# Kernel optimization log

Hardware: AMD Instinct MI355X
Metric: run time of the kernel (lower is better)

The kernel has to match this reference:

```python
import jax, jax.numpy as jnp
import numpy as np


def _hilbert_d2xy(n, d):
    # standard Hilbert curve: distance d -> (x, y) on n x n grid (n power of 2)
    x = y = 0
    t = d
    s = 1
    while s < n:
        rx = 1 & (t // 2)
        ry = 1 & (t ^ rx)
        if ry == 0:
            if rx == 1:
                x = s - 1 - x
                y = s - 1 - y
            x, y = y, x
        x += s * rx
        y += s * ry
        t //= 4
        s *= 2
    return x, y


def _hilbert_perm(seq_len):
    n = int(round(np.sqrt(seq_len)))
    assert n * n == seq_len
    perm = np.empty(seq_len, dtype=np.int32)
    for d in range(seq_len):
        x, y = _hilbert_d2xy(n, d)
        perm[d] = y * n + x  # linear (row-major) index visited at Hilbert step d
    return perm


def setup_inputs() -> dict:
    key = jax.random.key(0)
    k1, k2, k3 = jax.random.split(key, 3)
    B, S, H, D = 1, 4096, 8, 64
    q = jax.random.normal(k1, (B, S, H, D), dtype=jnp.float32)
    k = jax.random.normal(k2, (B, S, H, D), dtype=jnp.float32)
    v = jax.random.normal(k3, (B, S, H, D), dtype=jnp.float32)
    hilbert_perm = jnp.asarray(_hilbert_perm(S))
    return {"q": q, "k": k, "v": v, "hilbert_perm": hilbert_perm}


def reference(q, k, v, hilbert_perm):
    B, S, H, D = q.shape
    inv_perm = jnp.argsort(hilbert_perm)

    # apply_hilbert_ordering along dim=1 (seq): gather by permutation
    q_o = q[:, hilbert_perm]
    k_o = k[:, hilbert_perm]
    v_o = v[:, hilbert_perm]

    # faithful to original: raw flat reshape of [B,S,H,D] -> [B*H, S, D]
    q_f = q_o.reshape(B * H, S, D)
    k_f = k_o.reshape(B * H, S, D)
    v_f = v_o.reshape(B * H, S, D)

    scale = 1.0 / jnp.sqrt(jnp.asarray(D, dtype=q.dtype))
    scores = jnp.einsum('bsd,btd->bst', q_f, k_f) * scale  # [B*H, S, S]
    attn = jax.nn.softmax(scores, axis=-1)
    out_f = jnp.einsum('bst,btd->bsd', attn, v_f)  # [B*H, S, D]

    out = out_f.reshape(B, H, S, D).transpose(0, 2, 1, 3).reshape(B, S, H, D)
    # inverse Hilbert ordering along dim=1
    return out[:, inv_perm]
```

## Files before the change

### kernel.cpp

```cpp
#include <hip/hip_runtime.h>

typedef _Float16 f16;
typedef _Float16 f16x4 __attribute__((ext_vector_type(4)));
typedef _Float16 f16x8 __attribute__((ext_vector_type(8)));
typedef __fp16 fp16x2 __attribute__((ext_vector_type(2)));
typedef float f32x4 __attribute__((ext_vector_type(4)));

#define MFMA_16x16x32_F16(A, B, C) __builtin_amdgcn_mfma_f32_16x16x32_f16((A), (B), (C), 0, 0, 0)

typedef const __attribute__((address_space(1))) char gchar;
typedef __attribute__((address_space(3))) char lchar;

__device__ __forceinline__ float fexp2(float x) { return __builtin_amdgcn_exp2f(x); }
__device__ __forceinline__ int swzb(int b) { return b ^ ((b >> 3) & 0x70); }

namespace {
constexpr int SB = 4096;
constexpr size_t BB = (size_t)SB * 64 * 2;
}

__global__ __launch_bounds__(256)
void hilbert_prepass_kernel(const float* __restrict__ kp, const float* __restrict__ vp,
                            const int* __restrict__ perm,
                            char* __restrict__ kw, char* __restrict__ vtw)
{
    const int bid = blockIdx.x;
    const int batch = bid & 7;
    const int tile = bid >> 3;
    const int tid = (int)threadIdx.x;
    const int r = tid >> 2;
    const int c4 = tid & 3;

    __shared__ float Vl[64][68];

    const int t = tile * 64 + r;
    const int srow = perm[batch * 512 + (t >> 3)];
    const size_t boff = (size_t)srow * 512 + (t & 7) * 64 + c4 * 16;

    {
        const float* ks = kp + boff;
        const float4 k0 = *(const float4*)(ks + 0);
        const float4 k1 = *(const float4*)(ks + 4);
        const float4 k2 = *(const float4*)(ks + 8);
        const float4 k3 = *(const float4*)(ks + 12);
        f16x8 h0, h1;
        h0[0] = (f16)k0.x; h0[1] = (f16)k0.y; h0[2] = (f16)k0.z; h0[3] = (f16)k0.w;
        h0[4] = (f16)k1.x; h0[5] = (f16)k1.y; h0[6] = (f16)k1.z; h0[7] = (f16)k1.w;
        h1[0] = (f16)k2.x; h1[1] = (f16)k2.y; h1[2] = (f16)k2.z; h1[3] = (f16)k2.w;
        h1[4] = (f16)k3.x; h1[5] = (f16)k3.y; h1[6] = (f16)k3.z; h1[7] = (f16)k3.w;
        char* kt = kw + (size_t)batch * BB + (size_t)tile * 8192;
        const int o = r * 128 + c4 * 32;
        *(f16x8*)(kt + swzb(o)) = h0;
        *(f16x8*)(kt + swzb(o + 16)) = h1;
    }
    {
        const float* vs = vp + boff;
        *(float4*)&Vl[r][c4 * 16 + 0]  = *(const float4*)(vs + 0);
        *(float4*)&Vl[r][c4 * 16 + 4]  = *(const float4*)(vs + 4);
        *(float4*)&Vl[r][c4 * 16 + 8]  = *(const float4*)(vs + 8);
        *(float4*)&Vl[r][c4 * 16 + 12] = *(const float4*)(vs + 12);
    }
    __syncthreads();
    {
        const int d = tid >> 2;
        const int tq = (tid & 3) * 16;
        f16x8 a, b;
#pragma unroll
        for (int j = 0; j < 8; ++j) a[j] = (f16)Vl[tq + j][d];
#pragma unroll
        for (int j = 0; j < 8; ++j) b[j] = (f16)Vl[tq + 8 + j][d];
        char* vt = vtw + (size_t)batch * BB + (size_t)tile * 8192;
        const int o = d * 128 + tq * 2;
        *(f16x8*)(vt + swzb(o)) = a;
        *(f16x8*)(vt + swzb(o + 16)) = b;
    }
}

__global__ __launch_bounds__(512, 2)
void hilbert_attn_kernel(const float* __restrict__ qp,
                         const int* __restrict__ perm,
                         const char* __restrict__ kw, const char* __restrict__ vtw,
                         float* __restrict__ op)
{
    __shared__ __align__(16) char SM[98304];

    const int bid = blockIdx.x;
    const int batch = bid & 7;
    const int qbase = (bid >> 3) * 128;
    const int tid = (int)threadIdx.x;
    const int w = tid >> 6;
    const int lane = tid & 63;
    const int l16 = lane & 15;
    const int g = lane >> 4;
    const int half = w >> 2;
    const int wq = w & 3;
    const int swz = (l16 & 7) << 4;

    f16x8 Qf0[2], Qf1[2];
    {
        constexpr float qscl = 0.125f * 1.44269504088896340736f;
#pragma unroll
        for (int s = 0; s < 2; ++s) {
            const int t = qbase + wq * 32 + s * 16 + l16;
            const int srow = perm[batch * 512 + (t >> 3)];
            const float* src = qp + (size_t)srow * 512 + (t & 7) * 64 + g * 8;
#pragma unroll
            for (int kt = 0; kt < 2; ++kt) {
                const float4 x0 = *(const float4*)(src + 32 * kt);
                const float4 x1 = *(const float4*)(src + 32 * kt + 4);
                f16x8 f;
                f[0] = (f16)(x0.x * qscl); f[1] = (f16)(x0.y * qscl);
                f[2] = (f16)(x0.z * qscl); f[3] = (f16)(x0.w * qscl);
                f[4] = (f16)(x1.x * qscl); f[5] = (f16)(x1.y * qscl);
                f[6] = (f16)(x1.z * qscl); f[7] = (f16)(x1.w * qscl);
                if (s == 0) Qf0[kt] = f; else Qf1[kt] = f;
            }
        }
    }

    f32x4 oacc0[4], oacc1[4];
#pragma unroll
    for (int i = 0; i < 4; ++i) {
        oacc0[i] = (f32x4){0.f, 0.f, 0.f, 0.f};
        oacc1[i] = (f32x4){0.f, 0.f, 0.f, 0.f};
    }
    float lr0 = 0.f, lr1 = 0.f;

    const char* ksrc = kw + (size_t)batch * BB + (size_t)tid * 16;
    const char* vsrc = vtw + (size_t)batch * BB + (size_t)tid * 16;
    char* pbase = &SM[65536 + w * 4096];

    {
        lchar* dst = (lchar*)&SM[w << 10];
        __builtin_amdgcn_global_load_lds((gchar*)(ksrc), dst, 16, 0, 0);
        __builtin_amdgcn_global_load_lds((gchar*)(ksrc + 8192), dst + 8192, 16, 0, 0);
        __builtin_amdgcn_global_load_lds((gchar*)(vsrc), dst + 16384, 16, 0, 0);
        __builtin_amdgcn_global_load_lds((gchar*)(vsrc + 8192), dst + 24576, 16, 0, 0);
    }
    __syncthreads();

    for (int it = 0; it < 32; ++it) {
        const int cur = it & 1;
        const int kbb = cur * 32768 + half * 8192;
        const int vbb = cur * 32768 + 16384 + half * 8192;

        if (it < 31) {
            const size_t go = (size_t)(it + 1) * 16384;
            lchar* dst = (lchar*)&SM[(cur ^ 1) * 32768 + (w << 10)];
            __builtin_amdgcn_global_load_lds((gchar*)(ksrc + go), dst, 16, 0, 0);
            __builtin_amdgcn_global_load_lds((gchar*)(ksrc + go + 8192), dst + 8192, 16, 0, 0);
            __builtin_amdgcn_global_load_lds((gchar*)(vsrc + go), dst + 16384, 16, 0, 0);
            __builtin_amdgcn_global_load_lds((gchar*)(vsrc + go + 8192), dst + 24576, 16, 0, 0);
        }

        f32x4 sa0[4], sa1[4];
#pragma unroll
        for (int i = 0; i < 4; ++i) {
            sa0[i] = (f32x4){0.f, 0.f, 0.f, 0.f};
            sa1[i] = (f32x4){0.f, 0.f, 0.f, 0.f};
        }
#pragma unroll
        for (int kt = 0; kt < 2; ++kt) {
#pragma unroll
            for (int mt = 0; mt < 4; ++mt) {
                const int off = kbb + (l16 + 16 * mt) * 128 + (((g + 4 * kt) * 16) ^ swz);
                const f16x8 kf = *(const f16x8*)&SM[off];
                sa0[mt] = MFMA_16x16x32_F16(kf, Qf0[kt], sa0[mt]);
                sa1[mt] = MFMA_16x16x32_F16(kf, Qf1[kt], sa1[mt]);
            }
        }

#pragma unroll
        for (int mt = 0; mt < 4; ++mt) {
            const float a0 = fexp2(sa0[mt][0]);
            const float a1 = fexp2(sa0[mt][1]);
            const float a2 = fexp2(sa0[mt][2]);
            const float a3 = fexp2(sa0[mt][3]);
            lr0 += (a0 + a1) + (a2 + a3);
            union { f16x4 v; fp16x2 h[2]; } u;
            u.h[0] = __builtin_amdgcn_cvt_pkrtz(a0, a1);
            u.h[1] = __builtin_amdgcn_cvt_pkrtz(a2, a3);
            const int poff = l16 * 128 + (((2 * mt + (g >> 1)) ^ (l16 & 7)) << 4) + (g & 1) * 8;
            *(f16x4*)&pbase[poff] = u.v;

            const float b0 = fexp2(sa1[mt][0]);
            const float b1 = fexp2(sa1[mt][1]);
            const float b2 = fexp2(sa1[mt][2]);
            const float b3 = fexp2(sa1[mt][3]);
            lr1 += (b0 + b1) + (b2 + b3);
            union { f16x4 v; fp16x2 h[2]; } u2;
            u2.h[0] = __builtin_amdgcn_cvt_pkrtz(b0, b1);
            u2.h[1] = __builtin_amdgcn_cvt_pkrtz(b2, b3);
            *(f16x4*)&pbase[2048 + poff] = u2.v;
        }

#pragma unroll
        for (int kt = 0; kt < 2; ++kt) {
            const int poff = l16 * 128 + (((g + 4 * kt) ^ (l16 & 7)) << 4);
            const f16x8 pf0 = *(const f16x8*)&pbase[poff];
            const f16x8 pf1 = *(const f16x8*)&pbase[2048 + poff];
#pragma unroll
            for (int mtd = 0; mtd < 4; ++mtd) {
                const int voff = vbb + (l16 + 16 * mtd) * 128 + (((g + 4 * kt) * 16) ^ swz);
                const f16x8 vf = *(const f16x8*)&SM[voff];
                oacc0[mtd] = MFMA_16x16x32_F16(vf, pf0, oacc0[mtd]);
                oacc1[mtd] = MFMA_16x16x32_F16(vf, pf1, oacc1[mtd]);
            }
        }

        __syncthreads();
    }

    lr0 += __shfl_xor(lr0, 16);
    lr0 += __shfl_xor(lr0, 32);
    lr1 += __shfl_xor(lr1, 16);
    lr1 += __shfl_xor(lr1, 32);

    float* OB = (float*)SM;
    float* ML = (float*)&SM[32768];
    if (w >= 4) {
        float* ob = OB + wq * 2048;
#pragma unroll
        for (int mtd = 0; mtd < 4; ++mtd) {
            *(f32x4*)&ob[l16 * 64 + mtd * 16 + g * 4] = oacc0[mtd];
            *(f32x4*)&ob[(16 + l16) * 64 + mtd * 16 + g * 4] = oacc1[mtd];
        }
        if (g == 0) {
            ML[wq * 32 + l16] = lr0;
            ML[wq * 32 + 16 + l16] = lr1;
        }
    }
    __syncthreads();
    if (w < 4) {
        float* ob = OB + wq * 2048;
#pragma unroll
        for (int s = 0; s < 2; ++s) {
            const float lmine = (s == 0) ? lr0 : lr1;
            const float linv = 1.f / (lmine + ML[wq * 32 + s * 16 + l16]);
            const int t = qbase + wq * 32 + s * 16 + l16;
            const int srow = perm[t];
            float* dst = op + (size_t)srow * 512 + batch * 64 + 4 * g;
#pragma unroll
            for (int mtd = 0; mtd < 4; ++mtd) {
                const f32x4 mine = (s == 0) ? oacc0[mtd] : oacc1[mtd];
                const f32x4 o2 = *(const f32x4*)&ob[(s * 16 + l16) * 64 + mtd * 16 + g * 4];
                float4 o;
                o.x = (mine[0] + o2[0]) * linv;
                o.y = (mine[1] + o2[1]) * linv;
                o.z = (mine[2] + o2[2]) * linv;
                o.w = (mine[3] + o2[3]) * linv;
                *(float4*)(dst + 16 * mtd) = o;
            }
        }
    }
}

extern "C" void kernel_launch(void* const* d_in, const int* in_sizes, int n_in,
                              void* d_out, int out_size, void* d_ws, size_t ws_size,
                              hipStream_t stream) {
    (void)in_sizes; (void)n_in; (void)out_size; (void)ws_size;
    const float* q = (const float*)d_in[0];
    const float* k = (const float*)d_in[1];
    const float* v = (const float*)d_in[2];
    const int* perm = (const int*)d_in[3];
    float* out = (float*)d_out;
    char* kw = (char*)d_ws;
    char* vtw = kw + 8 * BB;
    hipLaunchKernelGGL(hilbert_prepass_kernel, dim3(512), dim3(256), 0, stream,
                       k, v, perm, kw, vtw);
    hipLaunchKernelGGL(hilbert_attn_kernel, dim3(256), dim3(512), 0, stream,
                       q, perm, kw, vtw, out);
}
```

Baseline: 56.74 us.

## Keep softmax probabilities in registers by permuting V layout to match MFMA output

The prepass now writes transposed V with its key dimension permuted, so the fp16 probability fragments produced from the QK MFMA accumulators can feed the PV MFMA directly as register operands. This removes the per-iteration LDS write and read of the P tile and shrinks shared memory from 96KB to 64KB per block. It also raises wave priority around the MFMA sections with s_setprio. The gain relies on the key permutation (kinv mapping) matching the accumulator lane layout exactly; a mismatch would give wrong results.

```diff
diff --git a/kernel.cpp b/kernel.cpp
--- a/kernel.cpp
+++ b/kernel.cpp
@@ -17,6 +17,10 @@
 namespace {
 constexpr int SB = 4096;
 constexpr size_t BB = (size_t)SB * 64 * 2;
+}
+
+__device__ __forceinline__ int kinv(int r) {
+    return 32 * (r >> 5) + 8 * ((r >> 2) & 3) + 4 * ((r >> 4) & 1) + (r & 3);
 }
 
 __global__ __launch_bounds__(256)
@@ -63,16 +67,16 @@
     __syncthreads();
     {
         const int d = tid >> 2;
-        const int tq = (tid & 3) * 16;
-        f16x8 a, b;
-#pragma unroll
-        for (int j = 0; j < 8; ++j) a[j] = (f16)Vl[tq + j][d];
-#pragma unroll
-        for (int j = 0; j < 8; ++j) b[j] = (f16)Vl[tq + 8 + j][d];
+        const int a = tid & 3;
         char* vt = vtw + (size_t)batch * BB + (size_t)tile * 8192;
-        const int o = d * 128 + tq * 2;
-        *(f16x8*)(vt + swzb(o)) = a;
-        *(f16x8*)(vt + swzb(o + 16)) = b;
+        const int b0 = 32 * (a >> 1) + 4 * (a & 1);
+#pragma unroll
+        for (int gp = 0; gp < 4; ++gp) {
+            f16x4 qv;
+#pragma unroll
+            for (int v = 0; v < 4; ++v) qv[v] = (f16)Vl[16 * a + 4 * gp + v][d];
+            *(f16x4*)(vt + swzb(d * 128 + (b0 + 8 * gp) * 2)) = qv;
+        }
     }
 }
 
@@ -82,7 +86,7 @@
                          const char* __restrict__ kw, const char* __restrict__ vtw,
                          float* __restrict__ op)
 {
-    __shared__ __align__(16) char SM[98304];
+    __shared__ __align__(16) char SM[65536];
 
     const int bid = blockIdx.x;
     const int batch = bid & 7;
@@ -128,7 +132,6 @@
 
     const char* ksrc = kw + (size_t)batch * BB + (size_t)tid * 16;
     const char* vsrc = vtw + (size_t)batch * BB + (size_t)tid * 16;
-    char* pbase = &SM[65536 + w * 4096];
 
     {
         lchar* dst = (lchar*)&SM[w << 10];
@@ -159,6 +162,7 @@
             sa0[i] = (f32x4){0.f, 0.f, 0.f, 0.f};
             sa1[i] = (f32x4){0.f, 0.f, 0.f, 0.f};
         }
+        __builtin_amdgcn_s_setprio(1);
 #pragma unroll
         for (int kt = 0; kt < 2; ++kt) {
 #pragma unroll
@@ -169,36 +173,35 @@
                 sa1[mt] = MFMA_16x16x32_F16(kf, Qf1[kt], sa1[mt]);
             }
         }
-
+        __builtin_amdgcn_s_setprio(0);
+
+        float e0[16], e1[16];
 #pragma unroll
         for (int mt = 0; mt < 4; ++mt) {
-            const float a0 = fexp2(sa0[mt][0]);
-            const float a1 = fexp2(sa0[mt][1]);
-            const float a2 = fexp2(sa0[mt][2]);
-            const float a3 = fexp2(sa0[mt][3]);
-            lr0 += (a0 + a1) + (a2 + a3);
-            union { f16x4 v; fp16x2 h[2]; } u;
-            u.h[0] = __builtin_amdgcn_cvt_pkrtz(a0, a1);
-            u.h[1] = __builtin_amdgcn_cvt_pkrtz(a2, a3);
-            const int poff = l16 * 128 + (((2 * mt + (g >> 1)) ^ (l16 & 7)) << 4) + (g & 1) * 8;
-            *(f16x4*)&pbase[poff] = u.v;
-
-            const float b0 = fexp2(sa1[mt][0]);
-            const float b1 = fexp2(sa1[mt][1]);
-            const float b2 = fexp2(sa1[mt][2]);
-            const float b3 = fexp2(sa1[mt][3]);
-            lr1 += (b0 + b1) + (b2 + b3);
-            union { f16x4 v; fp16x2 h[2]; } u2;
-            u2.h[0] = __builtin_amdgcn_cvt_pkrtz(b0, b1);
-            u2.h[1] = __builtin_amdgcn_cvt_pkrtz(b2, b3);
-            *(f16x4*)&pbase[2048 + poff] = u2.v;
-        }
-
+#pragma unroll
+            for (int v = 0; v < 4; ++v) {
+                e0[4 * mt + v] = fexp2(sa0[mt][v]);
+                e1[4 * mt + v] = fexp2(sa1[mt][v]);
+            }
+        }
+#pragma unroll
+        for (int i = 0; i < 16; ++i) { lr0 += e0[i]; lr1 += e1[i]; }
+
+        union U8 { f16x8 v; fp16x2 h[4]; };
+        U8 p0k0, p0k1, p1k0, p1k1;
+#pragma unroll
+        for (int i = 0; i < 4; ++i) {
+            p0k0.h[i] = __builtin_amdgcn_cvt_pkrtz(e0[2 * i], e0[2 * i + 1]);
+            p0k1.h[i] = __builtin_amdgcn_cvt_pkrtz(e0[8 + 2 * i], e0[9 + 2 * i]);
+            p1k0.h[i] = __builtin_amdgcn_cvt_pkrtz(e1[2 * i], e1[2 * i + 1]);
+            p1k1.h[i] = __builtin_amdgcn_cvt_pkrtz(e1[8 + 2 * i], e1[9 + 2 * i]);
+        }
+
+        __builtin_amdgcn_s_setprio(1);
 #pragma unroll
         for (int kt = 0; kt < 2; ++kt) {
-            const int poff = l16 * 128 + (((g + 4 * kt) ^ (l16 & 7)) << 4);
-            const f16x8 pf0 = *(const f16x8*)&pbase[poff];
-            const f16x8 pf1 = *(const f16x8*)&pbase[2048 + poff];
+            const f16x8 pf0 = kt ? p0k1.v : p0k0.v;
+            const f16x8 pf1 = kt ? p1k1.v : p1k0.v;
 #pragma unroll
             for (int mtd = 0; mtd < 4; ++mtd) {
                 const int voff = vbb + (l16 + 16 * mtd) * 128 + (((g + 4 * kt) * 16) ^ swz);
@@ -207,6 +210,7 @@
                 oacc1[mtd] = MFMA_16x16x32_F16(vf, pf1, oacc1[mtd]);
             }
         }
+        __builtin_amdgcn_s_setprio(0);
 
         __syncthreads();
     }
```

Result: faster. 51.95 us (-8.5%).
